# Kernel tuning notes

Hardware: AMD Instinct MI355X
Metric: run time of the kernel (lower is better)

The kernel has to match this reference:

```python
import jax, jax.numpy as jnp
import numpy as np

LSP_ORDER = 32
RATE = 0.01
N_ITER = 4
MIN_D = RATE * np.pi / (LSP_ORDER + 1)  # _precompute


def setup_inputs() -> dict:
    key = jax.random.key(0)
    # LSP coefficients in radians, valid range (0, pi)
    w = jax.random.uniform(key, (256, 4096, LSP_ORDER + 1), dtype=jnp.float32,
                           minval=0.0, maxval=float(np.pi))
    return {"w": w}


def reference(w):
    min_d = jnp.asarray(MIN_D, w.dtype)
    pi = jnp.asarray(np.pi, w.dtype)
    K, w1 = w[..., :1], w[..., 1:]  # (..., 1), (..., M)

    def one_pass(w1):
        # Sequential left-to-right repair: each pair (m, m+1) is pushed apart
        # by half the deficit; the updated right element feeds the next step.
        wt = jnp.moveaxis(w1, -1, 0)  # (M, ...)

        def step(c, nxt):
            s = 0.5 * jnp.maximum(min_d - (nxt - c), 0.0)
            return nxt + s, c - s  # carry = updated w1[m+1], out = final w1[m]

        c_last, outs = jax.lax.scan(step, wt[0], wt[1:])
        w1n = jnp.concatenate([outs, c_last[None]], axis=0)  # (M, ...)
        return jnp.clip(jnp.moveaxis(w1n, 0, -1), min_d, pi - min_d)

    # Early-exit break in the original is a no-op once converged (step sizes
    # become 0 and clip is idempotent), so running all N_ITER is exact.
    for _ in range(N_ITER):
        w1 = one_pass(w1)

    return jnp.concatenate([K, w1], axis=-1)
```

## Files before the change

### kernel.cpp

```cpp
#include <hip/hip_runtime.h>
#include <math.h>


#define THREADS 64
#define ROW 33
#define TROWS 64
#define FPT (TROWS * ROW)
#define V4PT (FPT / 4)
#define TAIL (V4PT - 8 * THREADS)
#define GRID 4096

typedef __attribute__((ext_vector_type(4))) float v4f;

__global__ __launch_bounds__(THREADS, 4) void lsp_stability_kernel(
    const float* __restrict__ in, float* __restrict__ out, int tiles)
{
    __shared__ alignas(16) float smem[FPT];
    const int tid = threadIdx.x;
    const int bid = blockIdx.x;
    if (bid >= tiles) return;
    const int grid = (int)gridDim.x;
    const int nt = (tiles - bid + grid - 1) / grid;

    const float MIND = (float)(0.01 * M_PI / 33.0);
    const float PI_F = (float)M_PI;
    const float HI = PI_F - MIND;

    v4f* s4 = (v4f*)smem;
    v4f r[9];

    {
        const v4f* g4 = (const v4f*)(in + (size_t)bid * FPT);
#pragma unroll
        for (int j = 0; j < 8; ++j)
            r[j] = __builtin_nontemporal_load(g4 + tid + j * THREADS);
        if (tid < TAIL)
            r[8] = __builtin_nontemporal_load(g4 + tid + 8 * THREADS);
    }

    for (int t = 0; t < nt; ++t) {
        const size_t tile = (size_t)bid + (size_t)t * grid;

#pragma unroll
        for (int j = 0; j < 8; ++j) s4[tid + j * THREADS] = r[j];
        if (tid < TAIL) s4[tid + 8 * THREADS] = r[8];

        if (t + 1 < nt) {
            const v4f* g4 = (const v4f*)(in + (tile + grid) * FPT);
#pragma unroll
            for (int j = 0; j < 8; ++j)
                r[j] = __builtin_nontemporal_load(g4 + tid + j * THREADS);
            if (tid < TAIL)
                r[8] = __builtin_nontemporal_load(g4 + tid + 8 * THREADS);
        }
        __builtin_amdgcn_sched_barrier(0);

        float w[32];
        float* row = smem + tid * ROW;
#pragma unroll
        for (int k = 0; k < 32; ++k) w[k] = row[k + 1];

#pragma unroll
        for (int it = 0; it < 4; ++it) {
            float c = w[0];
#pragma unroll
            for (int k = 1; k < 32; ++k) {
                float nxt = w[k];
                float sft = 0.5f * fmaxf(MIND - (nxt - c), 0.0f);
                w[k - 1] = c - sft;
                c = nxt + sft;
            }
            w[31] = c;
#pragma unroll
            for (int k = 0; k < 32; ++k)
                w[k] = fminf(fmaxf(w[k], MIND), HI);
        }

#pragma unroll
        for (int k = 0; k < 32; ++k) row[k + 1] = w[k];

        v4f* out4 = (v4f*)(out + tile * FPT);
#pragma unroll
        for (int j = 0; j < 8; ++j)
            out4[tid + j * THREADS] = s4[tid + j * THREADS];
        if (tid < TAIL)
            out4[tid + 8 * THREADS] = s4[tid + 8 * THREADS];
    }
}

extern "C" void kernel_launch(void* const* d_in, const int* in_sizes, int n_in,
                              void* d_out, int out_size, void* d_ws, size_t ws_size,
                              hipStream_t stream) {
    const float* in = (const float*)d_in[0];
    float* out = (float*)d_out;
    const int tiles = in_sizes[0] / FPT;
    const int blocks = tiles < GRID ? tiles : GRID;
    lsp_stability_kernel<<<blocks, THREADS, 0, stream>>>(in, out, tiles);
}
```

Measured before the change: 227.8 us.

## Replace persistent prefetching grid with one block per tile

Removes the persistent-block loop that prefetched the next tile into registers while computing the current one, and launches one 64-thread block per tile instead. It also drops the minimum-blocks launch bound. The intent is to rely on hardware occupancy rather than manual register prefetch to hide memory latency, freeing registers. It risks losing the explicit load/compute overlap and adds per-block scheduling overhead.

```diff
diff --git a/kernel.cpp b/kernel.cpp
--- a/kernel.cpp
+++ b/kernel.cpp
@@ -8,84 +8,64 @@
 #define FPT (TROWS * ROW)
 #define V4PT (FPT / 4)
 #define TAIL (V4PT - 8 * THREADS)
-#define GRID 4096
 
 typedef __attribute__((ext_vector_type(4))) float v4f;
 
-__global__ __launch_bounds__(THREADS, 4) void lsp_stability_kernel(
-    const float* __restrict__ in, float* __restrict__ out, int tiles)
+__global__ __launch_bounds__(THREADS) void lsp_stability_kernel(
+    const float* __restrict__ in, float* __restrict__ out)
 {
     __shared__ alignas(16) float smem[FPT];
     const int tid = threadIdx.x;
-    const int bid = blockIdx.x;
-    if (bid >= tiles) return;
-    const int grid = (int)gridDim.x;
-    const int nt = (tiles - bid + grid - 1) / grid;
+    const size_t base = (size_t)blockIdx.x * FPT;
 
     const float MIND = (float)(0.01 * M_PI / 33.0);
     const float PI_F = (float)M_PI;
     const float HI = PI_F - MIND;
 
     v4f* s4 = (v4f*)smem;
-    v4f r[9];
-
     {
-        const v4f* g4 = (const v4f*)(in + (size_t)bid * FPT);
+        const v4f* g4 = (const v4f*)(in + base);
+        v4f r[9];
 #pragma unroll
         for (int j = 0; j < 8; ++j)
             r[j] = __builtin_nontemporal_load(g4 + tid + j * THREADS);
         if (tid < TAIL)
             r[8] = __builtin_nontemporal_load(g4 + tid + 8 * THREADS);
-    }
-
-    for (int t = 0; t < nt; ++t) {
-        const size_t tile = (size_t)bid + (size_t)t * grid;
-
 #pragma unroll
         for (int j = 0; j < 8; ++j) s4[tid + j * THREADS] = r[j];
         if (tid < TAIL) s4[tid + 8 * THREADS] = r[8];
+    }
 
-        if (t + 1 < nt) {
-            const v4f* g4 = (const v4f*)(in + (tile + grid) * FPT);
+    float w[32];
+    float* row = smem + tid * ROW;
 #pragma unroll
-            for (int j = 0; j < 8; ++j)
-                r[j] = __builtin_nontemporal_load(g4 + tid + j * THREADS);
-            if (tid < TAIL)
-                r[8] = __builtin_nontemporal_load(g4 + tid + 8 * THREADS);
-        }
-        __builtin_amdgcn_sched_barrier(0);
-
-        float w[32];
-        float* row = smem + tid * ROW;
-#pragma unroll
-        for (int k = 0; k < 32; ++k) w[k] = row[k + 1];
+    for (int k = 0; k < 32; ++k) w[k] = row[k + 1];
 
 #pragma unroll
-        for (int it = 0; it < 4; ++it) {
-            float c = w[0];
+    for (int it = 0; it < 4; ++it) {
+        float c = w[0];
 #pragma unroll
-            for (int k = 1; k < 32; ++k) {
-                float nxt = w[k];
-                float sft = 0.5f * fmaxf(MIND - (nxt - c), 0.0f);
-                w[k - 1] = c - sft;
-                c = nxt + sft;
-            }
-            w[31] = c;
+        for (int k = 1; k < 32; ++k) {
+            float nxt = w[k];
+            float sft = 0.5f * fmaxf(MIND - (nxt - c), 0.0f);
+            w[k - 1] = c - sft;
+            c = nxt + sft;
+        }
+        w[31] = c;
 #pragma unroll
-            for (int k = 0; k < 32; ++k)
-                w[k] = fminf(fmaxf(w[k], MIND), HI);
-        }
+        for (int k = 0; k < 32; ++k)
+            w[k] = fminf(fmaxf(w[k], MIND), HI);
+    }
 
 #pragma unroll
-        for (int k = 0; k < 32; ++k) row[k + 1] = w[k];
+    for (int k = 0; k < 32; ++k) row[k + 1] = w[k];
 
-        v4f* out4 = (v4f*)(out + tile * FPT);
+    v4f* out4 = (v4f*)(out + base);
 #pragma unroll
-        for (int j = 0; j < 8; ++j)
-            out4[tid + j * THREADS] = s4[tid + j * THREADS];
-        if (tid < TAIL)
-            out4[tid + 8 * THREADS] = s4[tid + 8 * THREADS];
-    }
+    for (int j = 0; j < 8; ++j)
+        out4[tid + j * THREADS] = s4[tid + j * THREADS];
+    if (tid < TAIL)
+        out4[tid + 8 * THREADS] = s4[tid + 8 * THREADS];
 }
 
 extern "C" void kernel_launch(void* const* d_in, const int* in_sizes, int n_in,
@@ -93,7 +73,6 @@
                               hipStream_t stream) {
     const float* in = (const float*)d_in[0];
     float* out = (float*)d_out;
-    const int tiles = in_sizes[0] / FPT;
-    const int blocks = tiles < GRID ? tiles : GRID;
-    lsp_stability_kernel<<<blocks, THREADS, 0, stream>>>(in, out, tiles);
+    const int blocks = in_sizes[0] / FPT;
+    lsp_stability_kernel<<<blocks, THREADS, 0, stream>>>(in, out);
 }
```

New measurement: 227.7 us. No clear change (-0.0%).
